# Performance work log

Measured on AMD Instinct MI355X. Metric: run time of the kernel, lower is better.

## Reference

```python
import jax, jax.numpy as jnp
import numpy as np

N = 50000   # nodes
D = 128     # hidden_dim
H = 8       # num_heads
DK = D // H # per-head dim
E = 1600000 # edges
L = 2       # n_layers
LN_EPS = 1e-5


def _layer_norm(x, g, b):
    m = jnp.mean(x, axis=-1, keepdims=True)
    v = jnp.mean(jnp.square(x - m), axis=-1, keepdims=True)
    return (x - m) * jax.lax.rsqrt(v + LN_EPS) * g + b


def _gt_layer(h, src, dst, Wq, bq, Wk, bk, Wv, bv, Wo, bo, W1, b1, W2, b2, g1, be1, g2, be2):
    n = h.shape[0]
    Q = (h @ Wq + bq).reshape(n, H, DK)
    K = (h @ Wk + bk).reshape(n, H, DK)
    V = (h @ Wv + bv).reshape(n, H, DK)
    # per-edge scaled dot-product score: K[src] . Q[dst]
    score = jnp.einsum('ehd,ehd->eh', K[src], Q[dst]) / np.sqrt(DK)
    score = jnp.exp(jnp.clip(score, -5.0, 5.0))            # [E,H]
    wV = jax.ops.segment_sum(V[src] * score[:, :, None], dst, num_segments=n)  # [N,H,DK]
    z = jax.ops.segment_sum(score, dst, num_segments=n)    # [N,H]
    attn = wV / (z[:, :, None] + 1e-6)                     # possible_empty-safe softmax
    h_att = attn.reshape(n, D) @ Wo + bo
    h = _layer_norm(h + h_att, g1, be1)                    # residual + LN
    ffn = jax.nn.relu(h @ W1 + b1) @ W2 + b2
    h = _layer_norm(h + ffn, g2, be2)                      # residual + LN
    return h


def setup_inputs() -> dict:
    key = jax.random.key(0)
    ks = jax.random.split(key, 16)
    s = 1.0 / np.sqrt(D)
    s2 = 1.0 / np.sqrt(2 * D)
    w = lambda k, shape, sc: jax.random.normal(k, shape, jnp.float32) * sc
    return {
        'h':   jax.random.normal(ks[0], (N, D), jnp.float32),
        'src': jax.random.randint(ks[1], (E,), 0, N),
        'dst': jax.random.randint(ks[2], (E,), 0, N),
        'Wq': w(ks[3], (L, D, D), s), 'bq': jnp.zeros((L, D), jnp.float32),
        'Wk': w(ks[4], (L, D, D), s), 'bk': jnp.zeros((L, D), jnp.float32),
        'Wv': w(ks[5], (L, D, D), s), 'bv': jnp.zeros((L, D), jnp.float32),
        'Wo': w(ks[6], (L, D, D), s), 'bo': jnp.zeros((L, D), jnp.float32),
        'W1': w(ks[7], (L, D, 2 * D), s), 'b1': jnp.zeros((L, 2 * D), jnp.float32),
        'W2': w(ks[8], (L, 2 * D, D), s2), 'b2': jnp.zeros((L, D), jnp.float32),
        'ln1_g': jnp.ones((L, D), jnp.float32), 'ln1_b': jnp.zeros((L, D), jnp.float32),
        'ln2_g': jnp.ones((L, D), jnp.float32), 'ln2_b': jnp.zeros((L, D), jnp.float32),
    }


def reference(h, src, dst, Wq, bq, Wk, bk, Wv, bv, Wo, bo, W1, b1, W2, b2, ln1_g, ln1_b, ln2_g, ln2_b):
    for l in range(L):
        h = _gt_layer(h, src, dst, Wq[l], bq[l], Wk[l], bk[l], Wv[l], bv[l],
                      Wo[l], bo[l], W1[l], b1[l], W2[l], b2[l],
                      ln1_g[l], ln1_b[l], ln2_g[l], ln2_b[l])
    return h
```

## Files before the change

### kernel.cpp

```cpp
#include <hip/hip_runtime.h>

#define NN 50000
#define DD 128
#define HH 8
#define EE 1600000
#define LL 2

typedef unsigned short u16;
typedef __attribute__((ext_vector_type(8))) __bf16 bf16x8;
typedef __attribute__((ext_vector_type(4))) float f32x4;
typedef __attribute__((ext_vector_type(2))) float f32x2;

__device__ __forceinline__ float bf2f(u16 u){
    return __uint_as_float(((unsigned int)u) << 16);
}
__device__ __forceinline__ u16 f2bf(float f){
    unsigned int x = __float_as_uint(f);
    x = x + 0x7fff + ((x >> 16) & 1);
    return (u16)(x >> 16);
}

__device__ __forceinline__ void async16(const u16* g, u16* l){
    __builtin_amdgcn_global_load_lds(
        (const __attribute__((address_space(1))) unsigned int*)(const void*)g,
        (__attribute__((address_space(3))) unsigned int*)(void*)l, 16, 0, 0);
}

#define FILL_SUB 128
#define PREP_BLOCKS (1024 + 6250 + 384 + 768)

__global__ __launch_bounds__(256) void prep_kernel(
        const int* __restrict__ dst, int* __restrict__ cnt,
        const float* __restrict__ h_in, u16* __restrict__ hb,
        const float* __restrict__ Wq, const float* __restrict__ Wk, const float* __restrict__ Wv,
        const float* __restrict__ bq, const float* __restrict__ bk, const float* __restrict__ bv,
        u16* __restrict__ WtQKV, float* __restrict__ bQKV,
        const float* __restrict__ Wo, const float* __restrict__ W1, const float* __restrict__ W2,
        u16* __restrict__ WtO, u16* __restrict__ WtF1, u16* __restrict__ WtF2){
    int b = blockIdx.x;
    if (b < 1024){
        int slice = b & 7;
        int sub = b >> 3;
        int lo = slice * (NN / 8), hi = lo + (NN / 8);
        for (int e = sub * 256 + threadIdx.x; e < EE; e += FILL_SUB * 256){
            int d = dst[e];
            if (d >= lo && d < hi) atomicAdd(&cnt[d], 1);
        }
        return;
    }
    b -= 1024;
    if (b < 6250){
        int i = b * 256 + threadIdx.x;
        if (i < NN * DD / 4){
            float4 v = ((const float4*)h_in)[i];
            ushort4 o;
            o.x = f2bf(v.x); o.y = f2bf(v.y); o.z = f2bf(v.z); o.w = f2bf(v.w);
            ((ushort4*)hb)[i] = o;
        }
        return;
    }
    b -= 6250;
    if (b < 384){
        int l = b / 192;
        int idx = (b % 192) * 256 + threadIdx.x;
        if (idx < 384 * 128){
            int n = idx >> 7, k = idx & 127;
            const float* W = (n < 128) ? Wq : (n < 256) ? Wk : Wv;
            int nc = n & 127;
            WtQKV[(size_t)l * 384 * 128 + idx] = f2bf(W[(size_t)l * 128 * 128 + k * 128 + nc]);
            if (k == 0){
                const float* bb = (n < 128) ? bq : (n < 256) ? bk : bv;
                bQKV[l * 384 + n] = bb[l * 128 + nc];
            }
        }
        return;
    }
    b -= 384;
    {
        int which = b / 256;
        int rem = b % 256;
        int l = rem / 128;
        int idx = (rem % 128) * 256 + threadIdx.x;
        const float* in; u16* out; int R, C;
        if (which == 0){ in = Wo; out = WtO; R = 128; C = 128; }
        else if (which == 1){ in = W1; out = WtF1; R = 128; C = 256; }
        else { in = W2; out = WtF2; R = 256; C = 128; }
        int total = R * C;
        if (idx < total){
            size_t mat = (size_t)l * total;
            int r = idx / C, c = idx % C;
            out[mat + (size_t)c * R + r] = f2bf(in[mat + idx]);
        }
    }
}

__global__ __launch_bounds__(1024) void scan_kernel(const int* __restrict__ cnt,
                                                    int* __restrict__ offs, int* __restrict__ cur){
    __shared__ int wsum[16];
    __shared__ int carry_s;
    __shared__ int ctot_s;
    int t = threadIdx.x, lane = t & 63, w = t >> 6;
    if (t == 0){ offs[0] = 0; cur[0] = 0; carry_s = 0; }
    __syncthreads();
    const int N4 = NN / 4;
    for (int base = 0; base < N4; base += 1024){
        int i4 = base + t;
        int4 x = (i4 < N4) ? ((const int4*)cnt)[i4] : make_int4(0, 0, 0, 0);
        int s1 = x.x, s2 = s1 + x.y, s3 = s2 + x.z, s4 = s3 + x.w;
        int v = s4;
        #pragma unroll
        for (int d = 1; d < 64; d <<= 1){ int u = __shfl_up(v, d); if (lane >= d) v += u; }
        if (lane == 63) wsum[w] = v;
        __syncthreads();
        if (t < 16){
            int sv = wsum[t];
            int iv = sv;
            #pragma unroll
            for (int d = 1; d < 16; d <<= 1){ int u = __shfl_up(iv, d); if (t >= d) iv += u; }
            wsum[t] = iv - sv;
            if (t == 15) ctot_s = iv;
        }
        __syncthreads();
        int excl = carry_s + wsum[w] + (v - s4);
        if (i4 < N4){
            int o = 4 * i4;
            offs[o + 1] = excl + s1;  cur[o + 1] = excl + s1;
            offs[o + 2] = excl + s2;  cur[o + 2] = excl + s2;
            offs[o + 3] = excl + s3;  cur[o + 3] = excl + s3;
            offs[o + 4] = excl + s4;  cur[o + 4] = excl + s4;
        }
        __syncthreads();
        if (t == 0) carry_s += ctot_s;
        __syncthreads();
    }
}

__global__ __launch_bounds__(256) void fill_kernel(const int* __restrict__ src, const int* __restrict__ dst,
                                                   int* __restrict__ cur, int* __restrict__ srcs){
    int slice = blockIdx.x & 7;
    int sub = blockIdx.x >> 3;
    int lo = slice * (NN / 8), hi = lo + (NN / 8);
    for (int e = sub * 256 + threadIdx.x; e < EE; e += FILL_SUB * 256){
        int d = dst[e];
        if (d >= lo && d < hi){
            int p = atomicAdd(&cur[d], 1);
            srcs[p] = src[e];
        }
    }
}

#define BM 128
#define LDC 136

__device__ __forceinline__ void stage_tile(const u16* __restrict__ A, const u16* __restrict__ Wt,
                                           u16* As, u16* Bs, int M, int K, int m0, int n0, int k0,
                                           int w, int lane){
    int lr = lane >> 3;
    int swz = ((lane & 7) ^ lr) * 8;
    #pragma unroll
    for (int p = 0; p < 4; p++){
        int s = p * 4 + w;
        int ga = m0 + s * 8 + lr;
        if (ga >= M) ga = M - 1;
        async16(A + (size_t)ga * K + k0 + swz, As + s * 512);
        async16(Wt + (size_t)(n0 + s * 8 + lr) * K + k0 + swz, Bs + s * 512);
    }
}

__device__ __forceinline__ void mfma_tiles(const u16* As, const u16* Bs, f32x4 (&acc)[4][4],
                                           int wm, int wn, int l15, int hi){
    #pragma unroll
    for (int ks = 0; ks < 2; ks++){
        bf16x8 a[4], b[4];
        int ca = ((ks * 4 + hi) ^ (l15 & 7)) * 8;
        #pragma unroll
        for (int i = 0; i < 4; i++){
            a[i] = *(const bf16x8*)(As + (wm * 64 + i * 16 + l15) * 64 + ca);
            b[i] = *(const bf16x8*)(Bs + (wn * 64 + i * 16 + l15) * 64 + ca);
        }
        #pragma unroll
        for (int mi = 0; mi < 4; mi++)
            #pragma unroll
            for (int ni = 0; ni < 4; ni++)
                acc[mi][ni] = __builtin_amdgcn_mfma_f32_16x16x32_bf16(a[mi], b[ni], acc[mi][ni], 0, 0, 0);
    }
}

#define GEMM_LOOP(K)                                                          \
    for (int k0 = 0; k0 < (K); k0 += 64){                                     \
        __syncthreads();                                                      \
        stage_tile(A, Wt, As, Bs, M, (K), m0, n0, k0, w, lane);               \
        asm volatile("s_waitcnt vmcnt(0)" ::: "memory");                      \
        __syncthreads();                                                      \
        mfma_tiles(As, Bs, acc, wm, wn, l15, hi);                             \
    }

template<int K>
__global__ __launch_bounds__(256) void gemm_direct(const u16* __restrict__ A, const u16* __restrict__ Wt,
                                                   const float* __restrict__ bias,
                                                   u16* __restrict__ out, int M, int N, int relu){
    __shared__ __align__(16) char smem[128 * LDC * 2];
    u16* As = (u16*)smem;
    u16* Bs = As + 8192;
    u16* Cs = (u16*)smem;

    int tid = threadIdx.x;
    int m0 = blockIdx.x * BM, n0 = blockIdx.y * 128;
    int lane = tid & 63, w = tid >> 6;
    int wm = w >> 1, wn = w & 1;
    int l15 = lane & 15, hi = lane >> 4;

    f32x4 acc[4][4];
    #pragma unroll
    for (int mi = 0; mi < 4; mi++)
        #pragma unroll
        for (int ni = 0; ni < 4; ni++)
            acc[mi][ni] = (f32x4){0.f, 0.f, 0.f, 0.f};

    GEMM_LOOP(K)

    __syncthreads();
    #pragma unroll
    for (int mi = 0; mi < 4; mi++)
        #pragma unroll
        for (int ni = 0; ni < 4; ni++){
            int col = wn * 64 + ni * 16 + l15;
            float bval = bias[n0 + col];
            #pragma unroll
            for (int j = 0; j < 4; j++){
                int rl = wm * 64 + mi * 16 + hi * 4 + j;
                float v = acc[mi][ni][j] + bval;
                if (relu) v = fmaxf(v, 0.f);
                Cs[rl * LDC + col] = f2bf(v);
            }
        }
    __syncthreads();
    int qrow = tid >> 4, quad = tid & 15;
    #pragma unroll
    for (int p = 0; p < 8; p++){
        int rl = p * 16 + qrow;
        int gr = m0 + rl;
        if (gr < M){
            uint4 v = *(const uint4*)(&Cs[rl * LDC + quad * 8]);
            *(uint4*)(out + (size_t)gr * N + n0 + quad * 8) = v;
        }
    }
}

__global__ __launch_bounds__(256) void gemm_qkv(const u16* __restrict__ A, const u16* __restrict__ Wt,
                                                const float* __restrict__ bias,
                                                u16* __restrict__ Qb, u16* __restrict__ Kb,
                                                unsigned char* __restrict__ Vb, int M){
    __shared__ __align__(16) char smem[128 * LDC * 2];
    u16* As = (u16*)smem;
    u16* Bs = As + 8192;
    u16* Cs = (u16*)smem;

    int tid = threadIdx.x;
    int m0 = blockIdx.x * BM, n0 = blockIdx.y * 128;
    int lane = tid & 63, w = tid >> 6;
    int wm = w >> 1, wn = w & 1;
    int l15 = lane & 15, hi = lane >> 4;

    f32x4 acc[4][4];
    #pragma unroll
    for (int mi = 0; mi < 4; mi++)
        #pragma unroll
        for (int ni = 0; ni < 4; ni++)
            acc[mi][ni] = (f32x4){0.f, 0.f, 0.f, 0.f};

    GEMM_LOOP(128)

    __syncthreads();
    #pragma unroll
    for (int mi = 0; mi < 4; mi++)
        #pragma unroll
        for (int ni = 0; ni < 4; ni++){
            int col = wn * 64 + ni * 16 + l15;
            float bval = bias[n0 + col];
            #pragma unroll
            for (int j = 0; j < 4; j++){
                int rl = wm * 64 + mi * 16 + hi * 4 + j;
                Cs[rl * LDC + col] = f2bf(acc[mi][ni][j] + bval);
            }
        }
    __syncthreads();
    int qrow = tid >> 4, quad = tid & 15;
    if (n0 < 256){
        u16* Tb = (n0 == 0) ? Qb : Kb;
        #pragma unroll
        for (int p = 0; p < 8; p++){
            int rl = p * 16 + qrow;
            int gr = m0 + rl;
            if (gr < M){
                uint4 v = *(const uint4*)(&Cs[rl * LDC + quad * 8]);
                *(uint4*)(Tb + (size_t)gr * 128 + quad * 8) = v;
            }
        }
    } else {
        #pragma unroll
        for (int p = 0; p < 8; p++){
            int rl = p * 16 + qrow;
            int gr = m0 + rl;
            if (gr < M){
                uint4 v = *(const uint4*)(&Cs[rl * LDC + quad * 8]);
                float f0 = bf2f((u16)(v.x & 0xffff)), f1 = bf2f((u16)(v.x >> 16));
                float f2 = bf2f((u16)(v.y & 0xffff)), f3 = bf2f((u16)(v.y >> 16));
                float f4 = bf2f((u16)(v.z & 0xffff)), f5 = bf2f((u16)(v.z >> 16));
                float f6 = bf2f((u16)(v.w & 0xffff)), f7 = bf2f((u16)(v.w >> 16));
                unsigned int w0 = __builtin_amdgcn_cvt_pk_fp8_f32(f0, f1, 0u, false);
                w0 = __builtin_amdgcn_cvt_pk_fp8_f32(f2, f3, w0, true);
                unsigned int w1 = __builtin_amdgcn_cvt_pk_fp8_f32(f4, f5, 0u, false);
                w1 = __builtin_amdgcn_cvt_pk_fp8_f32(f6, f7, w1, true);
                *(uint2*)(Vb + (size_t)gr * 128 + quad * 8) = make_uint2(w0, w1);
            }
        }
    }
}

template<int K>
__global__ __launch_bounds__(256) void gemm_ln(const u16* __restrict__ A, const u16* __restrict__ Wt,
                                               const float* __restrict__ bias, const u16* __restrict__ resid,
                                               const float* __restrict__ g, const float* __restrict__ b,
                                               u16* __restrict__ out_bf, float* __restrict__ out_f,
                                               int M){
    __shared__ __align__(16) u16 As[8192];
    __shared__ __align__(16) u16 Bs[8192];
    __shared__ float ps[2][128];
    __shared__ float pss[2][128];

    int tid = threadIdx.x;
    int m0 = blockIdx.x * BM;
    const int n0 = 0;
    int lane = tid & 63, w = tid >> 6;
    int wm = w >> 1, wn = w & 1;
    int l15 = lane & 15, hi = lane >> 4;

    f32x4 acc[4][4];
    #pragma unroll
    for (int mi = 0; mi < 4; mi++)
        #pragma unroll
        for (int ni = 0; ni < 4; ni++)
            acc[mi][ni] = (f32x4){0.f, 0.f, 0.f, 0.f};

    GEMM_LOOP(K)

    float gcol[4], bcol[4], bval[4];
    #pragma unroll
    for (int ni = 0; ni < 4; ni++){
        int col = wn * 64 + ni * 16 + l15;
        gcol[ni] = g[col]; bcol[ni] = b[col]; bval[ni] = bias[col];
    }

    #pragma unroll
    for (int mi = 0; mi < 4; mi++)
        #pragma unroll
        for (int j = 0; j < 4; j++){
            int rl = wm * 64 + mi * 16 + hi * 4 + j;
            int gr = m0 + rl;
            float s = 0.f, ss = 0.f;
            #pragma unroll
            for (int ni = 0; ni < 4; ni++){
                int col = wn * 64 + ni * 16 + l15;
                float x = acc[mi][ni][j] + bval[ni];
                if (gr < M) x += bf2f(resid[(size_t)gr * 128 + col]);
                acc[mi][ni][j] = x;
                s += x; ss += x * x;
            }
            #pragma unroll
            for (int d = 1; d < 16; d <<= 1){
                s  += __shfl_xor(s, d);
                ss += __shfl_xor(ss, d);
            }
            if (l15 == 0){ ps[wn][rl] = s; pss[wn][rl] = ss; }
        }
    __syncthreads();

    #pragma unroll
    for (int mi = 0; mi < 4; mi++)
        #pragma unroll
        for (int j = 0; j < 4; j++){
            int rl = wm * 64 + mi * 16 + hi * 4 + j;
            int gr = m0 + rl;
            if (gr >= M) continue;
            float s = ps[0][rl] + ps[1][rl];
            float ss = pss[0][rl] + pss[1][rl];
            float mean = s * (1.f / 128.f);
            float var = ss * (1.f / 128.f) - mean * mean;
            float r = rsqrtf(var + 1e-5f);
            #pragma unroll
            for (int ni = 0; ni < 4; ni++){
                int col = wn * 64 + ni * 16 + l15;
                float o = (acc[mi][ni][j] - mean) * r * gcol[ni] + bcol[ni];
                if (out_f) out_f[(size_t)gr * 128 + col] = o;
                else       out_bf[(size_t)gr * 128 + col] = f2bf(o);
            }
        }
}

__global__ __launch_bounds__(256) void edge_attn_kernel(const u16* __restrict__ Qb,
                                                        const u16* __restrict__ Kb,
                                                        const unsigned char* __restrict__ Vb,
                                                        const int* __restrict__ srcs,
                                                        const int* __restrict__ offs,
                                                        u16* __restrict__ att){
    int n = blockIdx.x * 4 + (threadIdx.x >> 6);
    if (n >= NN) return;
    int lane = threadIdx.x & 63;
    int laneh = lane & 31;
    int half = lane >> 5;

    float q0, q1, q2, q3;
    {
        uint2 qv = *(const uint2*)(Qb + (size_t)n * 128 + 4 * laneh);
        q0 = bf2f((u16)(qv.x & 0xffff)); q1 = bf2f((u16)(qv.x >> 16));
        q2 = bf2f((u16)(qv.y & 0xffff)); q3 = bf2f((u16)(qv.y >> 16));
    }
    const u16* kbase = Kb + 4 * laneh;
    const unsigned char* vbase = Vb + 4 * laneh;

    float w0 = 0.f, w1 = 0.f, w2 = 0.f, w3 = 0.f, z = 0.f;
    const float CS = 0.25f * 1.44269504f;

    auto proc = [&](uint2 kk, unsigned int vv, float gate){
        float k0 = bf2f((u16)(kk.x & 0xffff)), k1 = bf2f((u16)(kk.x >> 16));
        float k2 = bf2f((u16)(kk.y & 0xffff)), k3 = bf2f((u16)(kk.y >> 16));
        float p = q0 * k0 + q1 * k1 + q2 * k2 + q3 * k3;
        p += __shfl_xor(p, 1);
        p += __shfl_xor(p, 2);
        p = __builtin_amdgcn_fmed3f(p, -20.f, 20.f);
        float sc = __builtin_amdgcn_exp2f(p * CS) * gate;
        f32x2 vl = __builtin_amdgcn_cvt_pk_f32_fp8(vv, false);
        f32x2 vh = __builtin_amdgcn_cvt_pk_f32_fp8(vv, true);
        w0 += sc * vl[0]; w1 += sc * vl[1]; w2 += sc * vh[0]; w3 += sc * vh[1];
        z += sc;
    };

    int e0 = offs[n], e1 = offs[n + 1];
    int i = e0;
    for (; i + 15 < e1; i += 16){
        int s[8];
        #pragma unroll
        for (int u = 0; u < 8; u++) s[u] = srcs[i + 2 * u + half];
        uint2 kk[8];
        unsigned int vv[8];
        #pragma unroll
        for (int u = 0; u < 8; u++){
            kk[u] = *(const uint2*)(kbase + (size_t)s[u] * 128);
            vv[u] = *(const unsigned int*)(vbase + (size_t)s[u] * 128);
        }
        #pragma unroll
        for (int u = 0; u < 8; u++) proc(kk[u], vv[u], 1.f);
    }
    for (; i + 1 < e1; i += 2){
        int s = srcs[i + half];
        proc(*(const uint2*)(kbase + (size_t)s * 128),
             *(const unsigned int*)(vbase + (size_t)s * 128), 1.f);
    }
    if (i < e1){
        int s = srcs[i];
        proc(*(const uint2*)(kbase + (size_t)s * 128),
             *(const unsigned int*)(vbase + (size_t)s * 128), half ? 0.f : 1.f);
    }

    w0 += __shfl_xor(w0, 32); w1 += __shfl_xor(w1, 32);
    w2 += __shfl_xor(w2, 32); w3 += __shfl_xor(w3, 32);
    z  += __shfl_xor(z, 32);

    if (!half){
        float inv = 1.f / (z + 1e-6f);
        unsigned int oA = (unsigned int)f2bf(w0 * inv) | ((unsigned int)f2bf(w1 * inv) << 16);
        unsigned int oB = (unsigned int)f2bf(w2 * inv) | ((unsigned int)f2bf(w3 * inv) << 16);
        *(uint2*)(att + (size_t)n * DD + 4 * laneh) = make_uint2(oA, oB);
    }
}

extern "C" void kernel_launch(void* const* d_in, const int* in_sizes, int n_in,
                              void* d_out, int out_size, void* d_ws, size_t ws_size,
                              hipStream_t stream){
    const float* h_in = (const float*)d_in[0];
    const int* src  = (const int*)d_in[1];
    const int* dst  = (const int*)d_in[2];
    const float* Wq = (const float*)d_in[3];
    const float* bq = (const float*)d_in[4];
    const float* Wk = (const float*)d_in[5];
    const float* bk = (const float*)d_in[6];
    const float* Wv = (const float*)d_in[7];
    const float* bv = (const float*)d_in[8];
    const float* Wo = (const float*)d_in[9];
    const float* bo = (const float*)d_in[10];
    const float* W1 = (const float*)d_in[11];
    const float* b1 = (const float*)d_in[12];
    const float* W2 = (const float*)d_in[13];
    const float* b2 = (const float*)d_in[14];
    const float* ln1_g = (const float*)d_in[15];
    const float* ln1_b = (const float*)d_in[16];
    const float* ln2_g = (const float*)d_in[17];
    const float* ln2_b = (const float*)d_in[18];
    float* outp = (float*)d_out;

    char* ws = (char*)d_ws;
    auto alloc = [&](size_t bytes) -> char* {
        char* p = ws;
        ws += (bytes + 255) & ~(size_t)255;
        return p;
    };
    int* cnt   = (int*)alloc((size_t)NN * 4);
    int* offs  = (int*)alloc((size_t)(NN + 1) * 4);
    int* cur   = (int*)alloc((size_t)(NN + 1) * 4);
    int* srcs  = (int*)alloc((size_t)EE * 4);
    u16* WtQKV = (u16*)alloc((size_t)LL * 384 * 128 * 2);
    float* bQKV = (float*)alloc((size_t)LL * 384 * 4);
    u16* WtO   = (u16*)alloc((size_t)LL * 128 * 128 * 2);
    u16* WtF1  = (u16*)alloc((size_t)LL * 256 * 128 * 2);
    u16* WtF2  = (u16*)alloc((size_t)LL * 128 * 256 * 2);
    u16* hb    = (u16*)alloc((size_t)NN * DD * 2);
    u16* Qb    = (u16*)alloc((size_t)NN * 128 * 2);
    u16* Kb    = (u16*)alloc((size_t)NN * 128 * 2);
    unsigned char* Vb = (unsigned char*)alloc((size_t)NN * 128);
    u16* ffm   = (u16*)alloc((size_t)NN * 256 * 2);
    u16* att   = (u16*)alloc((size_t)NN * DD * 2);
    u16* h1    = (u16*)alloc((size_t)NN * DD * 2);
    u16* hmid  = (u16*)alloc((size_t)NN * DD * 2);

    hipMemsetAsync(cnt, 0, (size_t)NN * 4, stream);
    prep_kernel<<<PREP_BLOCKS, 256, 0, stream>>>(dst, cnt, h_in, hb,
                                                 Wq, Wk, Wv, bq, bk, bv, WtQKV, bQKV,
                                                 Wo, W1, W2, WtO, WtF1, WtF2);
    scan_kernel<<<1, 1024, 0, stream>>>(cnt, offs, cur);
    fill_kernel<<<8 * FILL_SUB, 256, 0, stream>>>(src, dst, cur, srcs);

    const int MB = (NN + BM - 1) / BM;
    const u16* hcur = hb;
    for (int l = 0; l < LL; l++){
        gemm_qkv<<<dim3(MB, 3), 256, 0, stream>>>(hcur, WtQKV + (size_t)l * 384 * 128,
                                                  bQKV + l * 384, Qb, Kb, Vb, NN);
        edge_attn_kernel<<<NN / 4, 256, 0, stream>>>(Qb, Kb, Vb, srcs, offs, att);
        gemm_ln<128><<<MB, 256, 0, stream>>>(att, WtO + (size_t)l * 128 * 128, bo + l * 128,
                                             hcur, ln1_g + l * 128, ln1_b + l * 128,
                                             h1, nullptr, NN);
        gemm_direct<128><<<dim3(MB, 2), 256, 0, stream>>>(h1, WtF1 + (size_t)l * 256 * 128,
                                                          b1 + l * 256, ffm, NN, 256, 1);
        if (l == LL - 1)
            gemm_ln<256><<<MB, 256, 0, stream>>>(ffm, WtF2 + (size_t)l * 128 * 256, b2 + l * 128,
                                                 h1, ln2_g + l * 128, ln2_b + l * 128,
                                                 nullptr, outp, NN);
        else
            gemm_ln<256><<<MB, 256, 0, stream>>>(ffm, WtF2 + (size_t)l * 128 * 256, b2 + l * 128,
                                                 h1, ln2_g + l * 128, ln2_b + l * 128,
                                                 hmid, nullptr, NN);
        hcur = hmid;
    }
}
```

Baseline: 485.7 us.

## Fuse FFN up-projection, ReLU, down-projection and LayerNorm into one kernel

```diff
diff --git a/kernel.cpp b/kernel.cpp
--- a/kernel.cpp
+++ b/kernel.cpp
@@ -195,58 +195,6 @@
         mfma_tiles(As, Bs, acc, wm, wn, l15, hi);                             \
     }
 
-template<int K>
-__global__ __launch_bounds__(256) void gemm_direct(const u16* __restrict__ A, const u16* __restrict__ Wt,
-                                                   const float* __restrict__ bias,
-                                                   u16* __restrict__ out, int M, int N, int relu){
-    __shared__ __align__(16) char smem[128 * LDC * 2];
-    u16* As = (u16*)smem;
-    u16* Bs = As + 8192;
-    u16* Cs = (u16*)smem;
-
-    int tid = threadIdx.x;
-    int m0 = blockIdx.x * BM, n0 = blockIdx.y * 128;
-    int lane = tid & 63, w = tid >> 6;
-    int wm = w >> 1, wn = w & 1;
-    int l15 = lane & 15, hi = lane >> 4;
-
-    f32x4 acc[4][4];
-    #pragma unroll
-    for (int mi = 0; mi < 4; mi++)
-        #pragma unroll
-        for (int ni = 0; ni < 4; ni++)
-            acc[mi][ni] = (f32x4){0.f, 0.f, 0.f, 0.f};
-
-    GEMM_LOOP(K)
-
-    __syncthreads();
-    #pragma unroll
-    for (int mi = 0; mi < 4; mi++)
-        #pragma unroll
-        for (int ni = 0; ni < 4; ni++){
-            int col = wn * 64 + ni * 16 + l15;
-            float bval = bias[n0 + col];
-            #pragma unroll
-            for (int j = 0; j < 4; j++){
-                int rl = wm * 64 + mi * 16 + hi * 4 + j;
-                float v = acc[mi][ni][j] + bval;
-                if (relu) v = fmaxf(v, 0.f);
-                Cs[rl * LDC + col] = f2bf(v);
-            }
-        }
-    __syncthreads();
-    int qrow = tid >> 4, quad = tid & 15;
-    #pragma unroll
-    for (int p = 0; p < 8; p++){
-        int rl = p * 16 + qrow;
-        int gr = m0 + rl;
-        if (gr < M){
-            uint4 v = *(const uint4*)(&Cs[rl * LDC + quad * 8]);
-            *(uint4*)(out + (size_t)gr * N + n0 + quad * 8) = v;
-        }
-    }
-}
-
 __global__ __launch_bounds__(256) void gemm_qkv(const u16* __restrict__ A, const u16* __restrict__ Wt,
                                                 const float* __restrict__ bias,
                                                 u16* __restrict__ Qb, u16* __restrict__ Kb,
@@ -318,12 +266,10 @@
     }
 }
 
-template<int K>
 __global__ __launch_bounds__(256) void gemm_ln(const u16* __restrict__ A, const u16* __restrict__ Wt,
                                                const float* __restrict__ bias, const u16* __restrict__ resid,
                                                const float* __restrict__ g, const float* __restrict__ b,
-                                               u16* __restrict__ out_bf, float* __restrict__ out_f,
-                                               int M){
+                                               u16* __restrict__ out_bf, int M){
     __shared__ __align__(16) u16 As[8192];
     __shared__ __align__(16) u16 Bs[8192];
     __shared__ float ps[2][128];
@@ -343,7 +289,7 @@
         for (int ni = 0; ni < 4; ni++)
             acc[mi][ni] = (f32x4){0.f, 0.f, 0.f, 0.f};
 
-    GEMM_LOOP(K)
+    GEMM_LOOP(128)
 
     float gcol[4], bcol[4], bval[4];
     #pragma unroll
@@ -392,6 +338,167 @@
             for (int ni = 0; ni < 4; ni++){
                 int col = wn * 64 + ni * 16 + l15;
                 float o = (acc[mi][ni][j] - mean) * r * gcol[ni] + bcol[ni];
+                out_bf[(size_t)gr * 128 + col] = f2bf(o);
+            }
+        }
+}
+
+__global__ __launch_bounds__(256) void ffn_ln_kernel(const u16* __restrict__ h1,
+                                                     const u16* __restrict__ W1t, const float* __restrict__ b1,
+                                                     const u16* __restrict__ W2t, const float* __restrict__ b2,
+                                                     const float* __restrict__ g, const float* __restrict__ b,
+                                                     u16* __restrict__ out_bf, float* __restrict__ out_f,
+                                                     int M){
+    __shared__ __align__(16) u16 As[4096];
+    __shared__ __align__(16) u16 Bs[16384];
+    __shared__ __align__(16) u16 mid[16384];
+    __shared__ float ps[2][64];
+    __shared__ float pss[2][64];
+
+    int tid = threadIdx.x, lane = tid & 63, w = tid >> 6;
+    int l15 = lane & 15, hi = lane >> 4;
+    int m0 = blockIdx.x * 64;
+    int lr = lane >> 3;
+    int swz = ((lane & 7) ^ lr) * 8;
+
+    f32x4 acc1[4][4];
+    #pragma unroll
+    for (int mi = 0; mi < 4; mi++)
+        #pragma unroll
+        for (int ni = 0; ni < 4; ni++)
+            acc1[mi][ni] = (f32x4){0.f, 0.f, 0.f, 0.f};
+
+    for (int kh = 0; kh < 2; kh++){
+        __syncthreads();
+        #pragma unroll
+        for (int p = 0; p < 2; p++){
+            int s = p * 4 + w;
+            int ga = m0 + s * 8 + lr;
+            if (ga >= M) ga = M - 1;
+            async16(h1 + (size_t)ga * 128 + kh * 64 + swz, As + s * 512);
+        }
+        #pragma unroll
+        for (int p = 0; p < 8; p++){
+            int s = p * 4 + w;
+            int row = s * 8 + lr;
+            async16(W1t + (size_t)row * 128 + kh * 64 + swz, Bs + s * 512);
+        }
+        asm volatile("s_waitcnt vmcnt(0)" ::: "memory");
+        __syncthreads();
+        #pragma unroll
+        for (int ks = 0; ks < 2; ks++){
+            int ca = ((ks * 4 + hi) ^ (l15 & 7)) * 8;
+            bf16x8 a[4], bb[4];
+            #pragma unroll
+            for (int i = 0; i < 4; i++){
+                a[i] = *(const bf16x8*)(As + (i * 16 + l15) * 64 + ca);
+                bb[i] = *(const bf16x8*)(Bs + (w * 64 + i * 16 + l15) * 64 + ca);
+            }
+            #pragma unroll
+            for (int mi = 0; mi < 4; mi++)
+                #pragma unroll
+                for (int ni = 0; ni < 4; ni++)
+                    acc1[mi][ni] = __builtin_amdgcn_mfma_f32_16x16x32_bf16(a[mi], bb[ni], acc1[mi][ni], 0, 0, 0);
+        }
+    }
+
+    #pragma unroll
+    for (int ni = 0; ni < 4; ni++){
+        float bv = b1[w * 64 + ni * 16 + l15];
+        int kcol = ni * 16 + l15;
+        #pragma unroll
+        for (int mi = 0; mi < 4; mi++)
+            #pragma unroll
+            for (int j = 0; j < 4; j++){
+                int row = mi * 16 + hi * 4 + j;
+                float v = fmaxf(acc1[mi][ni][j] + bv, 0.f);
+                mid[w * 4096 + row * 64 + (((kcol >> 3) ^ (row & 7)) * 8 + (kcol & 7))] = f2bf(v);
+            }
+    }
+
+    int wm = w >> 1, wn = w & 1;
+    f32x4 acc2[2][4];
+    #pragma unroll
+    for (int mi = 0; mi < 2; mi++)
+        #pragma unroll
+        for (int ni = 0; ni < 4; ni++)
+            acc2[mi][ni] = (f32x4){0.f, 0.f, 0.f, 0.f};
+
+    for (int kt = 0; kt < 4; kt++){
+        __syncthreads();
+        #pragma unroll
+        for (int p = 0; p < 4; p++){
+            int s = p * 4 + w;
+            int row = s * 8 + lr;
+            async16(W2t + (size_t)row * 256 + kt * 64 + swz, Bs + s * 512);
+        }
+        asm volatile("s_waitcnt vmcnt(0)" ::: "memory");
+        __syncthreads();
+        #pragma unroll
+        for (int ks = 0; ks < 2; ks++){
+            int ca = ((ks * 4 + hi) ^ (l15 & 7)) * 8;
+            bf16x8 a[2], bb[4];
+            #pragma unroll
+            for (int i = 0; i < 2; i++)
+                a[i] = *(const bf16x8*)(mid + kt * 4096 + (wm * 32 + i * 16 + l15) * 64 + ca);
+            #pragma unroll
+            for (int i = 0; i < 4; i++)
+                bb[i] = *(const bf16x8*)(Bs + (wn * 64 + i * 16 + l15) * 64 + ca);
+            #pragma unroll
+            for (int mi = 0; mi < 2; mi++)
+                #pragma unroll
+                for (int ni = 0; ni < 4; ni++)
+                    acc2[mi][ni] = __builtin_amdgcn_mfma_f32_16x16x32_bf16(a[mi], bb[ni], acc2[mi][ni], 0, 0, 0);
+        }
+    }
+
+    float gcol[4], bcol[4], bval[4];
+    #pragma unroll
+    for (int ni = 0; ni < 4; ni++){
+        int col = wn * 64 + ni * 16 + l15;
+        gcol[ni] = g[col]; bcol[ni] = b[col]; bval[ni] = b2[col];
+    }
+
+    #pragma unroll
+    for (int mi = 0; mi < 2; mi++)
+        #pragma unroll
+        for (int j = 0; j < 4; j++){
+            int row = wm * 32 + mi * 16 + hi * 4 + j;
+            int gr = m0 + row;
+            float s = 0.f, ss = 0.f;
+            #pragma unroll
+            for (int ni = 0; ni < 4; ni++){
+                int col = wn * 64 + ni * 16 + l15;
+                float x = acc2[mi][ni][j] + bval[ni];
+                if (gr < M) x += bf2f(h1[(size_t)gr * 128 + col]);
+                acc2[mi][ni][j] = x;
+                s += x; ss += x * x;
+            }
+            #pragma unroll
+            for (int d = 1; d < 16; d <<= 1){
+                s  += __shfl_xor(s, d);
+                ss += __shfl_xor(ss, d);
+            }
+            if (l15 == 0){ ps[wn][row] = s; pss[wn][row] = ss; }
+        }
+    __syncthreads();
+
+    #pragma unroll
+    for (int mi = 0; mi < 2; mi++)
+        #pragma unroll
+        for (int j = 0; j < 4; j++){
+            int row = wm * 32 + mi * 16 + hi * 4 + j;
+            int gr = m0 + row;
+            if (gr >= M) continue;
+            float s = ps[0][row] + ps[1][row];
+            float ss = pss[0][row] + pss[1][row];
+            float mean = s * (1.f / 128.f);
+            float var = ss * (1.f / 128.f) - mean * mean;
+            float r = rsqrtf(var + 1e-5f);
+            #pragma unroll
+            for (int ni = 0; ni < 4; ni++){
+                int col = wn * 64 + ni * 16 + l15;
+                float o = (acc2[mi][ni][j] - mean) * r * gcol[ni] + bcol[ni];
                 if (out_f) out_f[(size_t)gr * 128 + col] = o;
                 else       out_bf[(size_t)gr * 128 + col] = f2bf(o);
             }
@@ -518,7 +625,6 @@
     u16* Qb    = (u16*)alloc((size_t)NN * 128 * 2);
     u16* Kb    = (u16*)alloc((size_t)NN * 128 * 2);
     unsigned char* Vb = (unsigned char*)alloc((size_t)NN * 128);
-    u16* ffm   = (u16*)alloc((size_t)NN * 256 * 2);
     u16* att   = (u16*)alloc((size_t)NN * DD * 2);
     u16* h1    = (u16*)alloc((size_t)NN * DD * 2);
     u16* hmid  = (u16*)alloc((size_t)NN * DD * 2);
@@ -531,24 +637,25 @@
     fill_kernel<<<8 * FILL_SUB, 256, 0, stream>>>(src, dst, cur, srcs);
 
     const int MB = (NN + BM - 1) / BM;
+    const int MB64 = (NN + 63) / 64;
     const u16* hcur = hb;
     for (int l = 0; l < LL; l++){
         gemm_qkv<<<dim3(MB, 3), 256, 0, stream>>>(hcur, WtQKV + (size_t)l * 384 * 128,
                                                   bQKV + l * 384, Qb, Kb, Vb, NN);
         edge_attn_kernel<<<NN / 4, 256, 0, stream>>>(Qb, Kb, Vb, srcs, offs, att);
-        gemm_ln<128><<<MB, 256, 0, stream>>>(att, WtO + (size_t)l * 128 * 128, bo + l * 128,
-                                             hcur, ln1_g + l * 128, ln1_b + l * 128,
-                                             h1, nullptr, NN);
-        gemm_direct<128><<<dim3(MB, 2), 256, 0, stream>>>(h1, WtF1 + (size_t)l * 256 * 128,
-                                                          b1 + l * 256, ffm, NN, 256, 1);
+        gemm_ln<<<MB, 256, 0, stream>>>(att, WtO + (size_t)l * 128 * 128, bo + l * 128,
+                                        hcur, ln1_g + l * 128, ln1_b + l * 128,
+                                        h1, NN);
         if (l == LL - 1)
-            gemm_ln<256><<<MB, 256, 0, stream>>>(ffm, WtF2 + (size_t)l * 128 * 256, b2 + l * 128,
-                                                 h1, ln2_g + l * 128, ln2_b + l * 128,
-                                                 nullptr, outp, NN);
+            ffn_ln_kernel<<<MB64, 256, 0, stream>>>(h1, WtF1 + (size_t)l * 256 * 128, b1 + l * 256,
+                                                    WtF2 + (size_t)l * 128 * 256, b2 + l * 128,
+                                                    ln2_g + l * 128, ln2_b + l * 128,
+                                                    nullptr, outp, NN);
         else
-            gemm_ln<256><<<MB, 256, 0, stream>>>(ffm, WtF2 + (size_t)l * 128 * 256, b2 + l * 128,
-                                                 h1, ln2_g + l * 128, ln2_b + l * 128,
-                                                 hmid, nullptr, NN);
+            ffn_ln_kernel<<<MB64, 256, 0, stream>>>(h1, WtF1 + (size_t)l * 256 * 128, b1 + l * 256,
+                                                    WtF2 + (size_t)l * 128 * 256, b2 + l * 128,
+                                                    ln2_g + l * 128, ln2_b + l * 128,
+                                                    hmid, nullptr, NN);
         hcur = hmid;
     }
 }
```

Measured after the change: 472.9 us. 1.03x faster.
